# Performance work log

Measured on AMD Instinct MI355X. Metric: run time of the kernel, lower is better.

The kernel has to match this reference:

```python
import jax, jax.numpy as jnp
import numpy as np

N = 100000
E = 1600000
IN_F = 64
HID = 128
GC_OUT = 128
FEATS_OUT = 128


def _init_params(key):
    ks = jax.random.split(key, 6)
    s = 0.02
    return dict(
        W1=jax.random.normal(ks[0], (IN_F, HID), jnp.float32) * s,
        b1=jnp.zeros((HID,), jnp.float32),
        W2=jax.random.normal(ks[1], (HID, HID), jnp.float32) * s,
        b2=jnp.zeros((HID,), jnp.float32),
        Wgc=jax.random.normal(ks[2], (HID + IN_F, GC_OUT), jnp.float32) * s,
        bgc=jnp.zeros((GC_OUT,), jnp.float32),
        Wc=jax.random.normal(ks[3], (HID + GC_OUT, FEATS_OUT), jnp.float32) * s,
        bc=jnp.zeros((FEATS_OUT,), jnp.float32),
    )


def setup_inputs() -> dict:
    key = jax.random.key(0)
    k_f, k_e, k_p = jax.random.split(key, 3)
    inp = dict(
        feats=jax.random.normal(k_f, (N, IN_F), jnp.float32),
        edges=jax.random.randint(k_e, (2, E), 0, N, jnp.int64 if jax.config.read('jax_enable_x64') else jnp.int32),
        batch=jnp.zeros((N,), jnp.int32),
    )
    inp.update(_init_params(k_p))
    return inp


def _gcn_conv(x, edges, Wgc, bgc):
    # PyG GCNConv: linear transform, add self-loops, symmetric deg norm, scatter-add.
    n = x.shape[0]
    x = x @ Wgc  # [N, GC_OUT]
    loop = jnp.arange(n, dtype=edges.dtype)
    src = jnp.concatenate([edges[0], loop])
    dst = jnp.concatenate([edges[1], loop])
    deg = jax.ops.segment_sum(jnp.ones_like(dst, dtype=x.dtype), dst, num_segments=n)
    dinv = jnp.where(deg > 0, jax.lax.rsqrt(deg), 0.0)
    norm = dinv[src] * dinv[dst]  # [E+N]
    msg = x[src] * norm[:, None]  # gather + scale (memory-bound)
    agg = jax.ops.segment_sum(msg, dst, num_segments=n)  # scatter-add
    return agg + bgc


def reference(feats, edges, batch, W1, b1, W2, b2, Wgc, bgc, Wc, bc):
    elu = jax.nn.elu
    nfeats = elu(elu(feats @ W1 + b1) @ W2 + b2)  # fcnn
    gc_in = jnp.concatenate([nfeats, feats], axis=1)  # inject_input_to_gc
    gc_feats = _gcn_conv(gc_in, edges, Wgc, bgc)
    out_feats = elu(jnp.concatenate([nfeats, gc_feats], axis=1) @ Wc + bc)
    return (out_feats, edges, batch)
```

## Files before the change

### kernel.cpp

```cpp
#include <hip/hip_runtime.h>
#include <hip/hip_bf16.h>
#include <hip/hip_fp8.h>

constexpr int NN = 100000;
constexpr int NE = 1600000;

constexpr int SH1  = 9;
constexpr int NB1  = (NN + 511) >> SH1;
constexpr int EB   = 8192;
constexpr int NBLK = (NE + EB - 1) / EB;
constexpr int NH   = NB1 * NBLK;

constexpr float FP8_SCL  = 128.f;
constexpr float FP8_ISCL = 1.f / 128.f;

typedef __bf16 bf16_t;
typedef bf16_t bf16x8 __attribute__((ext_vector_type(8)));
typedef bf16_t bf16x4 __attribute__((ext_vector_type(4)));
typedef float  f32x4  __attribute__((ext_vector_type(4)));
typedef float  f32x2  __attribute__((ext_vector_type(2)));

__device__ inline float elu_fast(float v) {
  return v > 0.f ? v : (__expf(v) - 1.f);
}

__device__ inline unsigned char f_to_fp8(float v) {
  __hip_fp8_e4m3 q(v);
  return q.__x;
}
template<int SEL>
__device__ inline float fp8_to_f(unsigned int word) {
#if __has_builtin(__builtin_amdgcn_cvt_f32_fp8)
  return __builtin_amdgcn_cvt_f32_fp8(word, SEL);
#else
  __hip_fp8_e4m3 t; t.__x = (word >> (8 * SEL)) & 0xff; return (float)t;
#endif
}
template<bool W>
__device__ inline f32x2 fp8pk2(unsigned int word) {
#if __has_builtin(__builtin_amdgcn_cvt_pk_f32_fp8)
  return __builtin_amdgcn_cvt_pk_f32_fp8((int)word, W);
#else
  f32x2 o; o.x = fp8_to_f<W ? 2 : 0>(word); o.y = fp8_to_f<W ? 3 : 1>(word); return o;
#endif
}
__device__ inline void fp8x8_add(float* acc, uint2 v) {
  f32x2 p0 = fp8pk2<false>(v.x);
  f32x2 p1 = fp8pk2<true >(v.x);
  f32x2 p2 = fp8pk2<false>(v.y);
  f32x2 p3 = fp8pk2<true >(v.y);
  acc[0] += p0.x; acc[1] += p0.y;
  acc[2] += p1.x; acc[3] += p1.y;
  acc[4] += p2.x; acc[5] += p2.y;
  acc[6] += p3.x; acc[7] += p3.y;
}
__device__ inline void fp8x8_fma(float* acc, uint2 v, float s) {
  f32x2 p0 = fp8pk2<false>(v.x);
  f32x2 p1 = fp8pk2<true >(v.x);
  f32x2 p2 = fp8pk2<false>(v.y);
  f32x2 p3 = fp8pk2<true >(v.y);
  acc[0] += p0.x * s; acc[1] += p0.y * s;
  acc[2] += p1.x * s; acc[3] += p1.y * s;
  acc[4] += p2.x * s; acc[5] += p2.y * s;
  acc[6] += p3.x * s; acc[7] += p3.y * s;
}

constexpr int SB = 256;

__global__ void scan_blk(const int* __restrict__ in, int* __restrict__ incl,
                         int* __restrict__ bsum, int n) {
  __shared__ int sm[SB];
  int i = blockIdx.x * SB + threadIdx.x;
  int v = (i < n) ? in[i] : 0;
  sm[threadIdx.x] = v;
  __syncthreads();
  for (int off = 1; off < SB; off <<= 1) {
    int t = (threadIdx.x >= off) ? sm[threadIdx.x - off] : 0;
    __syncthreads();
    sm[threadIdx.x] += t;
    __syncthreads();
  }
  if (i < n) incl[i] = sm[threadIdx.x];
  if (threadIdx.x == SB - 1) bsum[blockIdx.x] = sm[SB - 1];
}

__global__ void scan_top(int* __restrict__ bsum, int nb) {
  __shared__ int sm[512];
  int t = threadIdx.x;
  int v = (t < nb) ? bsum[t] : 0;
  sm[t] = v;
  __syncthreads();
  for (int off = 1; off < 512; off <<= 1) {
    int u = (t >= off) ? sm[t - off] : 0;
    __syncthreads();
    sm[t] += u;
    __syncthreads();
  }
  if (t < nb) bsum[t] = sm[t] - v;
}

__global__ void scan_add(const int* __restrict__ incl, const int* __restrict__ in,
                         const int* __restrict__ bsum, int* __restrict__ outoff, int n) {
  int i = blockIdx.x * SB + threadIdx.x;
  if (i < n) {
    int off = bsum[blockIdx.x];
    outoff[i] = off + incl[i] - in[i];
    if (i == n - 1) outoff[n] = off + incl[i];
  }
}


__global__ __launch_bounds__(256) void histA(const int* __restrict__ dst,
                                             int* __restrict__ H, int e) {
  __shared__ int h[NB1];
  for (int i = threadIdx.x; i < NB1; i += 256) h[i] = 0;
  __syncthreads();
  int base = blockIdx.x * EB;
  int end = min(base + EB, e);
  for (int i = base + threadIdx.x; i < end; i += 256)
    atomicAdd(&h[dst[i] >> SH1], 1);
  __syncthreads();
  for (int i = threadIdx.x; i < NB1; i += 256)
    H[i * NBLK + blockIdx.x] = h[i];
}

__global__ void boff_k(const int* __restrict__ Hoff, int* __restrict__ boff) {
  int i = blockIdx.x * blockDim.x + threadIdx.x;
  if (i < NB1) boff[i] = Hoff[i * NBLK];
  if (i == NB1) boff[NB1] = NE;
}

__global__ __launch_bounds__(256) void scatterA(
    const int* __restrict__ src, const int* __restrict__ dst,
    const int* __restrict__ Hoff, unsigned long long* __restrict__ ebuf, int e) {
  __shared__ int cur[NB1];
  for (int i = threadIdx.x; i < NB1; i += 256)
    cur[i] = Hoff[i * NBLK + blockIdx.x];
  __syncthreads();
  int base = blockIdx.x * EB;
  int end = min(base + EB, e);
  for (int i = base + threadIdx.x; i < end; i += 256) {
    int d = dst[i], s = src[i];
    int pos = atomicAdd(&cur[d >> SH1], 1);
    ebuf[pos] = ((unsigned long long)(unsigned)d << 32) | (unsigned)s;
  }
}


__global__ __launch_bounds__(512) void bfin(const unsigned long long* __restrict__ ebuf,
                                            const int* __restrict__ boff,
                                            int* __restrict__ row_off, float* __restrict__ dinv,
                                            int* __restrict__ csr, int n) {
  __shared__ int cnt[512];
  __shared__ int loc[512];
  const int tid = threadIdx.x;
  const int b = blockIdx.x;
  cnt[tid] = 0;
  __syncthreads();
  const int e0 = boff[b], e1 = boff[b + 1];
  for (int e = e0 + tid; e < e1; e += 512)
    atomicAdd(&cnt[(int)(ebuf[e] >> 32) & 511], 1);
  __syncthreads();
  loc[tid] = cnt[tid];
  __syncthreads();
  for (int off = 1; off < 512; off <<= 1) {
    int t = (tid >= off) ? loc[tid - off] : 0;
    __syncthreads();
    loc[tid] += t;
    __syncthreads();
  }
  const int excl = loc[tid] - cnt[tid];
  const int node = (b << SH1) + tid;
  if (node < n) {
    row_off[node] = boff[b] + excl;
    dinv[node] = rsqrtf((float)cnt[tid] + 1.0f);
  }
  if (b == NB1 - 1 && tid == 0) row_off[n] = NE;
  cnt[tid] = boff[b] + excl;
  __syncthreads();
  for (int e = e0 + tid; e < e1; e += 512) {
    unsigned long long v = ebuf[e];
    int dl = (int)(v >> 32) & 511;
    int s  = (int)(v & 0xffffffffu);
    int slot = atomicAdd(&cnt[dl], 1);
    csr[slot] = s;
  }
}


__global__ void i2f4_k(const int4* __restrict__ in, float4* __restrict__ out, int n4) {
  int i = blockIdx.x * blockDim.x + threadIdx.x;
  if (i < n4) {
    int4 v = in[i];
    out[i] = make_float4((float)v.x, (float)v.y, (float)v.z, (float)v.w);
  }
}

__global__ void wprep4(const float* __restrict__ W1, const float* __restrict__ W2,
                       const float* __restrict__ Wgc, const float* __restrict__ Wc,
                       bf16_t* __restrict__ Wf) {
  int idx = blockIdx.x * blockDim.x + threadIdx.x;
  const float* W; int base;
  if      (idx < 8192)  { W = W1;  base = 0; }
  else if (idx < 24576) { W = W2;  base = 8192; }
  else if (idx < 49152) { W = Wgc; base = 24576; }
  else                  { W = Wc;  base = 49152; }
  int il   = idx - base;
  int j    = il & 7;
  int lane = (il >> 3) & 63;
  int c    = (il >> 9) & 7;
  int kt   = il >> 12;
  int k    = kt * 32 + (lane >> 4) * 8 + j;
  int col  = c * 16 + (lane & 15);
  Wf[idx] = (bf16_t)W[(size_t)k * 128 + col];
}

__global__ __launch_bounds__(256) void mf_dense123(
    const float* __restrict__ A, const bf16_t* __restrict__ Wall,
    const float* __restrict__ b1, const float* __restrict__ b2,
    const float* __restrict__ dinv_g,
    bf16_t* __restrict__ h2out, unsigned char* __restrict__ xqout, int n)
{
  __shared__ __align__(16) char h1s[64 * 256];
  __shared__ __align__(16) char wbuf[16384];
  const int tid  = threadIdx.x;
  const int wv   = tid >> 6;
  const int lane = tid & 63;
  const int r    = lane & 15;
  const int kb   = lane >> 4;
  const int row0 = blockIdx.x * 64 + wv * 16;

  f32x4 acc[8];
  #pragma unroll
  for (int c = 0; c < 8; ++c) acc[c] = (f32x4){0.f, 0.f, 0.f, 0.f};

  int rowA = row0 + r; if (rowA >= n) rowA = n - 1;
  const int rloc = wv * 16 + r;

  for (int ch = 0; ch < 6; ++ch) {
    __syncthreads();
    {
      const char* src = (const char*)Wall + ch * 16384;
      #pragma unroll
      for (int k = 0; k < 4; ++k) {
        float4 v = *(const float4*)(src + k * 4096 + tid * 16);
        *(float4*)(wbuf + k * 4096 + tid * 16) = v;
      }
    }
    __syncthreads();

    #pragma unroll
    for (int lk = 0; lk < 2; ++lk) {
      const int gkt = ch * 2 + lk;
      bf16x8 a;
      if (gkt < 2) {
        const float* fp = A + (size_t)rowA * 64 + gkt * 32 + kb * 8;
        float4 u = *(const float4*)fp;
        float4 v = *(const float4*)(fp + 4);
        a = (bf16x8){(bf16_t)u.x, (bf16_t)u.y, (bf16_t)u.z, (bf16_t)u.w,
                     (bf16_t)v.x, (bf16_t)v.y, (bf16_t)v.z, (bf16_t)v.w};
      } else if (gkt < 6) {
        int kbyte = ((gkt - 2) * 32 + kb * 8) * 2;
        int off = (rloc * 256 + kbyte) ^ ((rloc & 7) << 4);
        a = *(const bf16x8*)(h1s + off);
      } else {
        int kofs = (gkt - 6) * 32 + kb * 8;
        if (kofs < 128) {
          int off = (rloc * 256 + kofs * 2) ^ ((rloc & 7) << 4);
          a = *(const bf16x8*)(h1s + off);
        } else {
          const float* fp = A + (size_t)rowA * 64 + (kofs - 128);
          float4 u = *(const float4*)fp;
          float4 v = *(const float4*)(fp + 4);
          a = (bf16x8){(bf16_t)u.x, (bf16_t)u.y, (bf16_t)u.z, (bf16_t)u.w,
                       (bf16_t)v.x, (bf16_t)v.y, (bf16_t)v.z, (bf16_t)v.w};
        }
      }
      #pragma unroll
      for (int c = 0; c < 8; ++c) {
        bf16x8 b = *(const bf16x8*)(wbuf + ((lk * 8 + c) * 64 + lane) * 16);
        acc[c] = __builtin_amdgcn_mfma_f32_16x16x32_bf16(a, b, acc[c], 0, 0, 0);
      }
      if (gkt == 1) {
        #pragma unroll
        for (int c = 0; c < 8; ++c) {
          const int col = c * 16 + r;
          const float bv = b1[col];
          #pragma unroll
          for (int q = 0; q < 4; ++q) {
            int rl = wv * 16 + kb * 4 + q;
            float v = elu_fast(acc[c][q] + bv);
            int off = (rl * 256 + col * 2) ^ ((rl & 7) << 4);
            *(bf16_t*)(h1s + off) = (bf16_t)v;
          }
          acc[c] = (f32x4){0.f, 0.f, 0.f, 0.f};
        }
      } else if (gkt == 5) {
        #pragma unroll
        for (int c = 0; c < 8; ++c) {
          const int col = c * 16 + r;
          const float bv = b2[col];
          #pragma unroll
          for (int q = 0; q < 4; ++q) {
            int row = row0 + kb * 4 + q;
            int rl  = wv * 16 + kb * 4 + q;
            float v = elu_fast(acc[c][q] + bv);
            int off = (rl * 256 + col * 2) ^ ((rl & 7) << 4);
            *(bf16_t*)(h1s + off) = (bf16_t)v;
            if (row < n) h2out[(size_t)row * 128 + col] = (bf16_t)v;
          }
          acc[c] = (f32x4){0.f, 0.f, 0.f, 0.f};
        }
      }
    }
  }

  float dv[4];
  #pragma unroll
  for (int q = 0; q < 4; ++q) {
    int row = row0 + kb * 4 + q;
    dv[q] = (row < n) ? dinv_g[row] * FP8_SCL : 0.f;
  }
  #pragma unroll
  for (int c = 0; c < 8; ++c) {
    const int col = c * 16 + r;
    #pragma unroll
    for (int q = 0; q < 4; ++q) {
      int row = row0 + kb * 4 + q;
      if (row < n)
        xqout[(size_t)row * 128 + col] = f_to_fp8(acc[c][q] * dv[q]);
    }
  }
}

__global__ __launch_bounds__(256) void mf_dense_s(
    const bf16_t* __restrict__ A1, const bf16_t* __restrict__ A2,
    const bf16_t* __restrict__ Wf, const float* __restrict__ bias,
    float* __restrict__ outf, int n)
{
  __shared__ __align__(16) char wbuf[16384];
  const int tid  = threadIdx.x;
  const int wv   = tid >> 6;
  const int lane = tid & 63;
  const int r    = lane & 15;
  const int kb   = lane >> 4;
  const int row0 = blockIdx.x * 64 + wv * 16;

  f32x4 acc[8];
  #pragma unroll
  for (int c = 0; c < 8; ++c) acc[c] = (f32x4){0.f, 0.f, 0.f, 0.f};

  int rowA = row0 + r; if (rowA >= n) rowA = n - 1;

  for (int ch = 0; ch < 4; ++ch) {
    __syncthreads();
    {
      const char* src = (const char*)Wf + ch * 16384;
      #pragma unroll
      for (int k = 0; k < 4; ++k) {
        float4 v = *(const float4*)(src + k * 4096 + tid * 16);
        *(float4*)(wbuf + k * 4096 + tid * 16) = v;
      }
    }
    __syncthreads();

    #pragma unroll
    for (int lk = 0; lk < 2; ++lk) {
      const int gkt = ch * 2 + lk;
      bf16x8 a;
      if (gkt < 4) a = *(const bf16x8*)(A1 + (size_t)rowA * 128 + gkt * 32 + kb * 8);
      else         a = *(const bf16x8*)(A2 + (size_t)rowA * 128 + (gkt - 4) * 32 + kb * 8);
      #pragma unroll
      for (int c = 0; c < 8; ++c) {
        bf16x8 b = *(const bf16x8*)(wbuf + ((lk * 8 + c) * 64 + lane) * 16);
        acc[c] = __builtin_amdgcn_mfma_f32_16x16x32_bf16(a, b, acc[c], 0, 0, 0);
      }
    }
  }

  #pragma unroll
  for (int c = 0; c < 8; ++c) {
    const int col = c * 16 + r;
    const float bv = bias[col];
    #pragma unroll
    for (int q = 0; q < 4; ++q) {
      int row = row0 + kb * 4 + q;
      if (row < n) {
        float v = elu_fast(acc[c][q] + bv);
        outf[(size_t)row * 128 + col] = v;
      }
    }
  }
}

__global__ __launch_bounds__(256) void gcn_agg6(
    const int* __restrict__ row_off, const int* __restrict__ csr,
    const float* __restrict__ dinv, const unsigned char* __restrict__ xq,
    const float* __restrict__ bgc, bf16_t* __restrict__ agg, int n)
{
  int w = (int)((blockIdx.x * (unsigned)blockDim.x + threadIdx.x) >> 6);
  if (w >= n) return;
  const int lane = threadIdx.x & 63;
  const int g  = lane >> 4;
  const int li = lane & 15;

  float acc[8];
  #pragma unroll
  for (int j = 0; j < 8; ++j) acc[j] = 0.f;

  if (g == 0) {
    uint2 sv = ((const uint2*)(xq + (size_t)w * 128))[li];
    fp8x8_add(acc, sv);
  }

  const int e0 = row_off[w], e1 = row_off[w + 1];
  int e = e0;
  for (; e + 16 <= e1; e += 16) {
    #pragma unroll
    for (int u = 0; u < 4; ++u) {
      int s = csr[e + 4 * u + g];
      uint2 v = ((const uint2*)(xq + (size_t)s * 128))[li];
      fp8x8_add(acc, v);
    }
  }
  for (; e < e1; e += 4) {
    int idx = e + g;
    int cidx = idx < e1 ? idx : e1 - 1;
    int s = csr[cidx];
    float coef = idx < e1 ? 1.f : 0.f;
    uint2 v = ((const uint2*)(xq + (size_t)s * 128))[li];
    fp8x8_fma(acc, v, coef);
  }

  #pragma unroll
  for (int j = 0; j < 8; ++j) {
    acc[j] += __shfl_xor(acc[j], 16);
    acc[j] += __shfl_xor(acc[j], 32);
  }

  if (g == 0) {
    const float sc = dinv[w] * FP8_ISCL;
    f32x4 b0 = ((const f32x4*)bgc)[2 * li];
    f32x4 b1 = ((const f32x4*)bgc)[2 * li + 1];
    bf16x8 o;
    o[0] = (bf16_t)(acc[0] * sc + b0[0]); o[1] = (bf16_t)(acc[1] * sc + b0[1]);
    o[2] = (bf16_t)(acc[2] * sc + b0[2]); o[3] = (bf16_t)(acc[3] * sc + b0[3]);
    o[4] = (bf16_t)(acc[4] * sc + b1[0]); o[5] = (bf16_t)(acc[5] * sc + b1[1]);
    o[6] = (bf16_t)(acc[6] * sc + b1[2]); o[7] = (bf16_t)(acc[7] * sc + b1[3]);
    ((bf16x8*)(agg + (size_t)w * 128))[li] = o;
  }
}


extern "C" void kernel_launch(void* const* d_in, const int* in_sizes, int n_in,
                              void* d_out, int out_size, void* d_ws, size_t ws_size,
                              hipStream_t stream) {
  (void)in_sizes; (void)n_in; (void)out_size; (void)ws_size;
  const float* feats = (const float*)d_in[0];
  const int*   edges = (const int*)d_in[1];
  const int*   batch = (const int*)d_in[2];
  const float* W1  = (const float*)d_in[3];
  const float* b1  = (const float*)d_in[4];
  const float* W2  = (const float*)d_in[5];
  const float* b2  = (const float*)d_in[6];
  const float* Wgc = (const float*)d_in[7];
  const float* bgc = (const float*)d_in[8];
  const float* Wc  = (const float*)d_in[9];
  const float* bc  = (const float*)d_in[10];
  float* out = (float*)d_out;

  bf16_t* h2b  = (bf16_t*)d_ws;
  bf16_t* aggb = h2b  + (size_t)NN * 128;
  unsigned char* xq8 = (unsigned char*)(aggb + (size_t)NN * 128);
  float*  dinv = (float*)(xq8 + (size_t)NN * 128);
  bf16_t* wall = (bf16_t*)(dinv + NN);
  bf16_t* wcf  = wall + 49152;

  int* scr     = (int*)d_out;
  int* csr_src = scr;
  int* row_off = csr_src + NE;
  int* H       = row_off + NN + 1;
  int* Hincl   = H + NH;
  int* Hoff    = Hincl + NH;
  int* boff    = Hoff + NH + 1;
  int* bsum2   = boff + NB1 + 1;
  unsigned long long* ebuf =
      (unsigned long long*)(((uintptr_t)(bsum2 + 512) + 7) & ~(uintptr_t)7);

  const int* esrc = edges;
  const int* edst = edges + NE;

  const int nscH = (NH + SB - 1) / SB;

  histA   <<<NBLK, 256, 0, stream>>>(edst, H, NE);
  scan_blk<<<nscH, SB, 0, stream>>>(H, Hincl, bsum2, NH);
  scan_top<<<1, 512, 0, stream>>>(bsum2, nscH);
  scan_add<<<nscH, SB, 0, stream>>>(Hincl, H, bsum2, Hoff, NH);
  boff_k  <<<1, 256, 0, stream>>>(Hoff, boff);
  scatterA<<<NBLK, 256, 0, stream>>>(esrc, edst, Hoff, ebuf, NE);
  bfin    <<<NB1, 512, 0, stream>>>(ebuf, boff, row_off, dinv, csr_src, NN);

  wprep4<<<320, 256, 0, stream>>>(W1, W2, Wgc, Wc, wall);

  const int nb = (NN + 63) / 64;
  mf_dense123<<<nb, 256, 0, stream>>>(feats, wall, b1, b2, dinv, h2b, xq8, NN);

  long long wthreads = (long long)NN * 64;
  gcn_agg6<<<(int)((wthreads + 255) / 256), 256, 0, stream>>>(
      row_off, csr_src, dinv, xq8, bgc, aggb, NN);

  mf_dense_s<<<nb, 256, 0, stream>>>(h2b, aggb, wcf, bc, out, NN);

  size_t off = (size_t)NN * 128;
  i2f4_k<<<(2 * NE / 4 + 255) / 256, 256, 0, stream>>>(
      (const int4*)edges, (float4*)(out + off), 2 * NE / 4);
  i2f4_k<<<(NN / 4 + 255) / 256, 256, 0, stream>>>(
      (const int4*)batch, (float4*)(out + off + (size_t)2 * NE), NN / 4);
}
```

Baseline: 177.3 us.

## Pack edge buffer to 32 bits, fuse small kernels, deepen aggregation gather unroll

```diff
diff --git a/kernel.cpp b/kernel.cpp
--- a/kernel.cpp
+++ b/kernel.cpp
@@ -99,13 +99,16 @@
   if (t < nb) bsum[t] = sm[t] - v;
 }
 
-__global__ void scan_add(const int* __restrict__ incl, const int* __restrict__ in,
-                         const int* __restrict__ bsum, int* __restrict__ outoff, int n) {
+__global__ void scan_add_h(const int* __restrict__ incl, const int* __restrict__ in,
+                           const int* __restrict__ bsum, int* __restrict__ Hoff,
+                           int* __restrict__ boff, int n) {
   int i = blockIdx.x * SB + threadIdx.x;
   if (i < n) {
     int off = bsum[blockIdx.x];
-    outoff[i] = off + incl[i] - in[i];
-    if (i == n - 1) outoff[n] = off + incl[i];
+    int ex = off + incl[i] - in[i];
+    Hoff[i] = ex;
+    if (i % NBLK == 0) boff[i / NBLK] = ex;
+    if (i == n - 1) { Hoff[n] = NE; boff[NB1] = NE; }
   }
 }
 
@@ -124,15 +127,9 @@
     H[i * NBLK + blockIdx.x] = h[i];
 }
 
-__global__ void boff_k(const int* __restrict__ Hoff, int* __restrict__ boff) {
-  int i = blockIdx.x * blockDim.x + threadIdx.x;
-  if (i < NB1) boff[i] = Hoff[i * NBLK];
-  if (i == NB1) boff[NB1] = NE;
-}
-
 __global__ __launch_bounds__(256) void scatterA(
     const int* __restrict__ src, const int* __restrict__ dst,
-    const int* __restrict__ Hoff, unsigned long long* __restrict__ ebuf, int e) {
+    const int* __restrict__ Hoff, unsigned int* __restrict__ ebuf, int e) {
   __shared__ int cur[NB1];
   for (int i = threadIdx.x; i < NB1; i += 256)
     cur[i] = Hoff[i * NBLK + blockIdx.x];
@@ -142,12 +139,12 @@
   for (int i = base + threadIdx.x; i < end; i += 256) {
     int d = dst[i], s = src[i];
     int pos = atomicAdd(&cur[d >> SH1], 1);
-    ebuf[pos] = ((unsigned long long)(unsigned)d << 32) | (unsigned)s;
-  }
-}
-
-
-__global__ __launch_bounds__(512) void bfin(const unsigned long long* __restrict__ ebuf,
+    ebuf[pos] = ((unsigned)(d & 511) << 17) | (unsigned)s;
+  }
+}
+
+
+__global__ __launch_bounds__(512) void bfin(const unsigned int* __restrict__ ebuf,
                                             const int* __restrict__ boff,
                                             int* __restrict__ row_off, float* __restrict__ dinv,
                                             int* __restrict__ csr, int n) {
@@ -159,7 +156,7 @@
   __syncthreads();
   const int e0 = boff[b], e1 = boff[b + 1];
   for (int e = e0 + tid; e < e1; e += 512)
-    atomicAdd(&cnt[(int)(ebuf[e] >> 32) & 511], 1);
+    atomicAdd(&cnt[ebuf[e] >> 17], 1);
   __syncthreads();
   loc[tid] = cnt[tid];
   __syncthreads();
@@ -179,21 +176,21 @@
   cnt[tid] = boff[b] + excl;
   __syncthreads();
   for (int e = e0 + tid; e < e1; e += 512) {
-    unsigned long long v = ebuf[e];
-    int dl = (int)(v >> 32) & 511;
-    int s  = (int)(v & 0xffffffffu);
+    unsigned int v = ebuf[e];
+    int dl = (int)(v >> 17);
+    int s  = (int)(v & 0x1FFFFu);
     int slot = atomicAdd(&cnt[dl], 1);
     csr[slot] = s;
   }
 }
 
 
-__global__ void i2f4_k(const int4* __restrict__ in, float4* __restrict__ out, int n4) {
+__global__ void i2f_all(const int4* __restrict__ e4, const int4* __restrict__ b4,
+                        float4* __restrict__ out, int ne4, int ntot4) {
   int i = blockIdx.x * blockDim.x + threadIdx.x;
-  if (i < n4) {
-    int4 v = in[i];
-    out[i] = make_float4((float)v.x, (float)v.y, (float)v.z, (float)v.w);
-  }
+  if (i >= ntot4) return;
+  int4 v = (i < ne4) ? e4[i] : b4[i - ne4];
+  out[i] = make_float4((float)v.x, (float)v.y, (float)v.z, (float)v.w);
 }
 
 __global__ void wprep4(const float* __restrict__ W1, const float* __restrict__ W2,
@@ -393,7 +390,7 @@
   }
 }
 
-__global__ __launch_bounds__(256) void gcn_agg6(
+__global__ __launch_bounds__(256) void gcn_agg8(
     const int* __restrict__ row_off, const int* __restrict__ csr,
     const float* __restrict__ dinv, const unsigned char* __restrict__ xq,
     const float* __restrict__ bgc, bf16_t* __restrict__ agg, int n)
@@ -415,15 +412,23 @@
 
   const int e0 = row_off[w], e1 = row_off[w + 1];
   int e = e0;
-  for (; e + 16 <= e1; e += 16) {
-    #pragma unroll
-    for (int u = 0; u < 4; ++u) {
-      int s = csr[e + 4 * u + g];
-      uint2 v = ((const uint2*)(xq + (size_t)s * 128))[li];
-      fp8x8_add(acc, v);
-    }
-  }
-  for (; e < e1; e += 4) {
+  for (; e + 32 <= e1; e += 32) {
+    int s[8];
+    #pragma unroll
+    for (int u = 0; u < 8; ++u) s[u] = csr[e + 4 * u + g];
+    uint2 v[8];
+    #pragma unroll
+    for (int u = 0; u < 8; ++u)
+      v[u] = ((const uint2*)(xq + (size_t)s[u] * 128))[li];
+    #pragma unroll
+    for (int u = 0; u < 8; ++u) fp8x8_add(acc, v[u]);
+  }
+  for (; e + 4 <= e1; e += 4) {
+    int s = csr[e + g];
+    uint2 v = ((const uint2*)(xq + (size_t)s * 128))[li];
+    fp8x8_add(acc, v);
+  }
+  if (e < e1) {
     int idx = e + g;
     int cidx = idx < e1 ? idx : e1 - 1;
     int s = csr[cidx];
@@ -484,21 +489,19 @@
   int* Hoff    = Hincl + NH;
   int* boff    = Hoff + NH + 1;
   int* bsum2   = boff + NB1 + 1;
-  unsigned long long* ebuf =
-      (unsigned long long*)(((uintptr_t)(bsum2 + 512) + 7) & ~(uintptr_t)7);
+  unsigned int* ebuf = (unsigned int*)(bsum2 + 512);
 
   const int* esrc = edges;
   const int* edst = edges + NE;
 
   const int nscH = (NH + SB - 1) / SB;
 
-  histA   <<<NBLK, 256, 0, stream>>>(edst, H, NE);
-  scan_blk<<<nscH, SB, 0, stream>>>(H, Hincl, bsum2, NH);
-  scan_top<<<1, 512, 0, stream>>>(bsum2, nscH);
-  scan_add<<<nscH, SB, 0, stream>>>(Hincl, H, bsum2, Hoff, NH);
-  boff_k  <<<1, 256, 0, stream>>>(Hoff, boff);
-  scatterA<<<NBLK, 256, 0, stream>>>(esrc, edst, Hoff, ebuf, NE);
-  bfin    <<<NB1, 512, 0, stream>>>(ebuf, boff, row_off, dinv, csr_src, NN);
+  histA     <<<NBLK, 256, 0, stream>>>(edst, H, NE);
+  scan_blk  <<<nscH, SB, 0, stream>>>(H, Hincl, bsum2, NH);
+  scan_top  <<<1, 512, 0, stream>>>(bsum2, nscH);
+  scan_add_h<<<nscH, SB, 0, stream>>>(Hincl, H, bsum2, Hoff, boff, NH);
+  scatterA  <<<NBLK, 256, 0, stream>>>(esrc, edst, Hoff, ebuf, NE);
+  bfin      <<<NB1, 512, 0, stream>>>(ebuf, boff, row_off, dinv, csr_src, NN);
 
   wprep4<<<320, 256, 0, stream>>>(W1, W2, Wgc, Wc, wall);
 
@@ -506,14 +509,13 @@
   mf_dense123<<<nb, 256, 0, stream>>>(feats, wall, b1, b2, dinv, h2b, xq8, NN);
 
   long long wthreads = (long long)NN * 64;
-  gcn_agg6<<<(int)((wthreads + 255) / 256), 256, 0, stream>>>(
+  gcn_agg8<<<(int)((wthreads + 255) / 256), 256, 0, stream>>>(
       row_off, csr_src, dinv, xq8, bgc, aggb, NN);
 
   mf_dense_s<<<nb, 256, 0, stream>>>(h2b, aggb, wcf, bc, out, NN);
 
   size_t off = (size_t)NN * 128;
-  i2f4_k<<<(2 * NE / 4 + 255) / 256, 256, 0, stream>>>(
-      (const int4*)edges, (float4*)(out + off), 2 * NE / 4);
-  i2f4_k<<<(NN / 4 + 255) / 256, 256, 0, stream>>>(
-      (const int4*)batch, (float4*)(out + off + (size_t)2 * NE), NN / 4);
-}
+  const int ne4 = 2 * NE / 4, ntot4 = (2 * NE + NN) / 4;
+  i2f_all<<<(ntot4 + 255) / 256, 256, 0, stream>>>(
+      (const int4*)edges, (const int4*)batch, (float4*)(out + off), ne4, ntot4);
+}
```

New measurement: 183.7 us. 1.04x slower.
